# Kernel optimization log

Measured on AMD Instinct MI355X. Metric: run time of the kernel, lower is better.

Reference implementation:

```python
import jax, jax.numpy as jnp
import numpy as np

B, C, H, W = 16, 1536, 32, 32
K = 64      # num_clusters
D = 128     # cluster_dim
T = 256     # token_dim
E = 2       # num_experts
SINK_ITERS = 3


def _l2n(x, axis):
    return x / jnp.maximum(jnp.linalg.norm(x, axis=axis, keepdims=True), 1e-12)


def setup_inputs() -> dict:
    key = jax.random.key(0)
    ks = jax.random.split(key, 16)
    w = lambda k, sh: (jax.random.normal(k, sh, jnp.float32) * 0.02)
    inp = {
        "x_feat": jax.random.normal(ks[0], (B, C, H, W), jnp.float32),
        "token": jax.random.normal(ks[1], (B, C), jnp.float32),
        # cluster_features: Conv1x1 C->512, ReLU, Conv1x1 512->D
        "cf_w1": w(ks[2], (512, C)), "cf_b1": jnp.zeros((512,), jnp.float32),
        "cf_w2": w(ks[3], (D, 512)), "cf_b2": jnp.zeros((D,), jnp.float32),
        # token_features: Linear C->512, ReLU, Linear 512->T
        "tf_w1": w(ks[4], (512, C)), "tf_b1": jnp.zeros((512,), jnp.float32),
        "tf_w2": w(ks[5], (T, 512)), "tf_b2": jnp.zeros((T,), jnp.float32),
        # MoE experts (stacked): Conv1x1 C->512, ReLU, Conv1x1 512->K
        "ex_w1": w(ks[6], (E, 512, C)), "ex_b1": jnp.zeros((E, 512), jnp.float32),
        "ex_w2": w(ks[7], (E, K, 512)), "ex_b2": jnp.zeros((E, K), jnp.float32),
        # gate: Linear C->128, ReLU, Linear 128->E
        "g_w1": w(ks[8], (128, C)), "g_b1": jnp.zeros((128,), jnp.float32),
        "g_w2": w(ks[9], (E, 128)), "g_b2": jnp.zeros((E,), jnp.float32),
        "dust_bin": jnp.array(1.0, jnp.float32),
    }
    return inp


def _log_optimal_transport(scores, alpha, iters):
    b, m, n = scores.shape
    ms, ns = jnp.float32(m), jnp.float32(n)
    bins = jnp.broadcast_to(alpha, (b, 1, n))
    Z = jnp.concatenate([scores, bins], axis=1)          # [b, m+1, n]
    norm = -jnp.log(ms + ns)
    log_mu = jnp.concatenate([jnp.full((m,), norm), (jnp.log(ns) + norm)[None]])
    log_nu = jnp.full((n,), norm)
    u = jnp.zeros((b, m + 1), Z.dtype)
    v = jnp.zeros((b, n), Z.dtype)
    for _ in range(iters):
        u = log_mu[None] - jax.nn.logsumexp(Z + v[:, None, :], axis=2)
        v = log_nu[None] - jax.nn.logsumexp(Z + u[:, :, None], axis=1)
    return Z + u[:, :, None] + v[:, None, :] - norm


def reference(x_feat, token, cf_w1, cf_b1, cf_w2, cf_b2, tf_w1, tf_b1, tf_w2,
              tf_b2, ex_w1, ex_b1, ex_w2, ex_b2, g_w1, g_b1, g_w2, g_b2,
              dust_bin):
    # dropout layers act as identity at inference
    xf = x_feat.reshape(B, C, H * W)                     # [B,C,N]
    # cluster features f: [B, D, N]
    h = jax.nn.relu(jnp.einsum('bcn,oc->bon', xf, cf_w1) + cf_b1[None, :, None])
    f = jnp.einsum('bon,do->bdn', h, cf_w2) + cf_b2[None, :, None]
    # MoE score p: [B, K, N]
    eh = jax.nn.relu(jnp.einsum('bcn,eoc->ebon', xf, ex_w1) + ex_b1[:, None, :, None])
    eo = jnp.einsum('ebon,eko->ebkn', eh, ex_w2) + ex_b2[:, None, :, None]
    g = jax.nn.relu(token @ g_w1.T + g_b1) @ g_w2.T + g_b2   # [B,E]
    gw = jax.nn.softmax(g, axis=1)
    p = jnp.einsum('be,ebkn->bkn', gw, eo)
    # token features t: [B, T]
    t = jax.nn.relu(token @ tf_w1.T + tf_b1) @ tf_w2.T + tf_b2
    # optimal transport + aggregation
    Z = _log_optimal_transport(p, dust_bin, SINK_ITERS)
    P = jnp.exp(Z)[:, :-1, :]                            # [B,K,N]
    agg = jnp.einsum('bdn,bkn->bdk', f, P)               # == (f*p).sum(-1)
    local = _l2n(agg, axis=1).reshape(B, D * K)
    out = jnp.concatenate([_l2n(t, axis=-1), local], axis=-1)
    return _l2n(out, axis=-1)
```

## Files before the change

### kernel.cpp

```cpp
#include <hip/hip_runtime.h>
#include <hip/hip_bf16.h>
#include <math.h>

#define B_  16
#define C_  1536
#define N_  1024
#define K_  64
#define D_  128
#define T_  256
#define OUTW (T_ + D_*K_)

typedef __attribute__((ext_vector_type(8))) short short8_t;
typedef __attribute__((ext_vector_type(4))) float f32x4;

__device__ __forceinline__ ushort f2bf(float f){
  union { float f; uint u; } x; x.f = f;
  return (ushort)((x.u + 0x7fffu + ((x.u >> 16) & 1u)) >> 16);
}

__device__ __forceinline__ void gload16(const ushort* g, ushort* l){
  __builtin_amdgcn_global_load_lds((const __attribute__((address_space(1))) void*)g,
                                   (__attribute__((address_space(3))) void*)l, 16, 0, 0);
}

__global__ __launch_bounds__(256) void k_prep_w(
    const float* __restrict__ cf_w1, const float* __restrict__ ex_w1,
    ushort* __restrict__ Wbf)
{
  size_t i = ((size_t)blockIdx.x*256 + threadIdx.x) * 8;
  const float* src = (i < (size_t)512*C_) ? (cf_w1 + i) : (ex_w1 + (i - (size_t)512*C_));
  float4 a = *(const float4*)(src);
  float4 b = *(const float4*)(src + 4);
  uint4 ov;
  ov.x = (uint)f2bf(a.x) | ((uint)f2bf(a.y) << 16);
  ov.y = (uint)f2bf(a.z) | ((uint)f2bf(a.w) << 16);
  ov.z = (uint)f2bf(b.x) | ((uint)f2bf(b.y) << 16);
  ov.w = (uint)f2bf(b.z) | ((uint)f2bf(b.w) << 16);
  *(uint4*)(Wbf + i) = ov;
}

__global__ __launch_bounds__(256) void k_prep_w2(
    const float* __restrict__ cf_w2, const float* __restrict__ ex_w2,
    ushort* __restrict__ W2bf)
{
  size_t i = ((size_t)blockIdx.x*256 + threadIdx.x) * 8;
  const float* src = (i < (size_t)65536) ? (cf_w2 + i) : (ex_w2 + (i - 65536));
  float4 a = *(const float4*)(src);
  float4 b = *(const float4*)(src + 4);
  uint4 ov;
  ov.x = (uint)f2bf(a.x) | ((uint)f2bf(a.y) << 16);
  ov.y = (uint)f2bf(a.z) | ((uint)f2bf(a.w) << 16);
  ov.z = (uint)f2bf(b.x) | ((uint)f2bf(b.y) << 16);
  ov.w = (uint)f2bf(b.z) | ((uint)f2bf(b.w) << 16);
  *(uint4*)(W2bf + i) = ov;
}

__global__ __launch_bounds__(256) void k_prep_x(
    const float* __restrict__ x, ushort* __restrict__ xT, int b0)
{
  const int bx = blockIdx.x;
  const int by = blockIdx.y;
  const int bz = blockIdx.z;
  const int t  = threadIdx.x;
  __shared__ float Ls[64][65];
  const float* xb = x + (size_t)(bz + b0)*C_*N_ + (size_t)by*64*N_ + bx*64;
  const int r  = t >> 4;
  const int cq = (t & 15) * 4;
  #pragma unroll
  for (int p = 0; p < 4; p++) {
    float4 v = *(const float4*)(xb + (size_t)(r + p*16)*N_ + cq);
    Ls[r + p*16][cq+0] = v.x; Ls[r + p*16][cq+1] = v.y;
    Ls[r + p*16][cq+2] = v.z; Ls[r + p*16][cq+3] = v.w;
  }
  __syncthreads();
  ushort* xTb = xT + ((size_t)bz*N_ + (size_t)bx*64)*C_ + by*64;
  const int rn = t >> 3;
  const int cc = (t & 7) * 8;
  #pragma unroll
  for (int p = 0; p < 2; p++) {
    int n = rn + p*32;
    uint4 ov;
    ov.x = (uint)f2bf(Ls[cc+0][n]) | ((uint)f2bf(Ls[cc+1][n]) << 16);
    ov.y = (uint)f2bf(Ls[cc+2][n]) | ((uint)f2bf(Ls[cc+3][n]) << 16);
    ov.z = (uint)f2bf(Ls[cc+4][n]) | ((uint)f2bf(Ls[cc+5][n]) << 16);
    ov.w = (uint)f2bf(Ls[cc+6][n]) | ((uint)f2bf(Ls[cc+7][n]) << 16);
    *(uint4*)(xTb + (size_t)n*C_ + cc) = ov;
  }
}

__global__ __launch_bounds__(256) void k_token_a(
    const float* __restrict__ token,
    const float* __restrict__ tf_w1, const float* __restrict__ tf_b1,
    const float* __restrict__ g_w1, const float* __restrict__ g_b1,
    float* __restrict__ th1, float* __restrict__ gh)
{
  const int b = blockIdx.y;
  const int o = blockIdx.x*4 + (threadIdx.x >> 6);
  const int lane = threadIdx.x & 63;
  const float* w; float bias; float* dst;
  if (o < 512) { w = tf_w1 + (size_t)o*C_; bias = tf_b1[o]; dst = th1 + b*512 + o; }
  else { int oo = o - 512; w = g_w1 + (size_t)oo*C_; bias = g_b1[oo]; dst = gh + b*128 + oo; }
  const float* tok = token + (size_t)b*C_;
  float s = 0.f;
  for (int c = lane; c < C_; c += 64) s = fmaf(tok[c], w[c], s);
  for (int off = 32; off; off >>= 1) s += __shfl_down(s, off);
  if (lane == 0) *dst = fmaxf(s + bias, 0.f);
}

__global__ __launch_bounds__(256) void k_token_b(
    const float* __restrict__ th1, const float* __restrict__ gh,
    const float* __restrict__ tf_w2, const float* __restrict__ tf_b2,
    const float* __restrict__ g_w2, const float* __restrict__ g_b2,
    float* __restrict__ tt, float* __restrict__ gw)
{
  const int b = blockIdx.y;
  const int wid = threadIdx.x >> 6, lane = threadIdx.x & 63;
  if (blockIdx.x < 64) {
    const int o = blockIdx.x*4 + wid;
    const float* w = tf_w2 + (size_t)o*512;
    const float* h = th1 + b*512;
    float s = 0.f;
    for (int c = lane; c < 512; c += 64) s = fmaf(h[c], w[c], s);
    for (int off = 32; off; off >>= 1) s += __shfl_down(s, off);
    if (lane == 0) tt[b*T_ + o] = s + tf_b2[o];
  } else {
    __shared__ float gl[2];
    if (wid < 2) {
      const float* w = g_w2 + wid*128;
      const float* h = gh + b*128;
      float s = 0.f;
      for (int c = lane; c < 128; c += 64) s = fmaf(h[c], w[c], s);
      for (int off = 32; off; off >>= 1) s += __shfl_down(s, off);
      if (lane == 0) gl[wid] = s + g_b2[wid];
    }
    __syncthreads();
    if (threadIdx.x == 0) {
      float m = fmaxf(gl[0], gl[1]);
      float e0 = __expf(gl[0]-m), e1 = __expf(gl[1]-m);
      float inv = 1.f / (e0 + e1);
      gw[b*2+0] = e0*inv; gw[b*2+1] = e1*inv;
    }
  }
}

__global__ __launch_bounds__(256) void k_gemm1(
    const ushort* __restrict__ Wbf, const ushort* __restrict__ xT,
    const float* __restrict__ cf_b1, const float* __restrict__ ex_b1,
    ushort* __restrict__ hT, int b0)
{
  const int bx = blockIdx.x;
  const int by = blockIdx.y;
  const int bz = blockIdx.z;
  const int t = threadIdx.x;
  const int wid = t >> 6, lane = t & 63;
  const int wr = wid >> 1, wc = wid & 1;
  __shared__ ushort Abuf[128*64];
  __shared__ ushort Bbuf[128*64];
  f32x4 acc[4][4];
  const f32x4 z4 = {0.f, 0.f, 0.f, 0.f};
  #pragma unroll
  for (int i = 0; i < 4; i++)
    #pragma unroll
    for (int j = 0; j < 4; j++) acc[i][j] = z4;

  const ushort* gA[4]; const ushort* gB[4];
  ushort* lA[4]; ushort* lB[4];
  #pragma unroll
  for (int j = 0; j < 4; j++) {
    int idx = j*256 + t;
    int row = idx >> 3, ps = idx & 7;
    int s = ps ^ (row & 7);
    gA[j] = Wbf + (size_t)(by*128 + row)*C_ + s*8;
    gB[j] = xT + ((size_t)bz*N_ + bx*128 + row)*C_ + s*8;
    lA[j] = &Abuf[(j*4 + wid)*512];
    lB[j] = &Bbuf[(j*4 + wid)*512];
  }

  for (int k0 = 0; k0 < C_; k0 += 64) {
    #pragma unroll
    for (int j = 0; j < 4; j++) {
      gload16(gA[j] + k0, lA[j]);
      gload16(gB[j] + k0, lB[j]);
    }
    __syncthreads();
    #pragma unroll
    for (int ks = 0; ks < 2; ks++) {
      short8_t a[4], bb[4];
      const int l15 = lane & 15, lg = lane >> 4;
      #pragma unroll
      for (int i = 0; i < 4; i++) {
        int row = wr*64 + i*16 + l15;
        int slot = ks*4 + lg;
        a[i] = *(const short8_t*)&Abuf[row*64 + ((slot ^ (row & 7)) * 8)];
      }
      #pragma unroll
      for (int j = 0; j < 4; j++) {
        int row = wc*64 + j*16 + l15;
        int slot = ks*4 + lg;
        bb[j] = *(const short8_t*)&Bbuf[row*64 + ((slot ^ (row & 7)) * 8)];
      }
      #pragma unroll
      for (int i = 0; i < 4; i++)
        #pragma unroll
        for (int j = 0; j < 4; j++)
          acc[i][j] = __builtin_amdgcn_mfma_f32_16x16x32_bf16(a[i], bb[j], acc[i][j], 0, 0, 0);
    }
    __syncthreads();
  }
  const int lr = lane >> 4, lc = lane & 15;
  #pragma unroll
  for (int i = 0; i < 4; i++) {
    int o4 = by*128 + wr*64 + i*16 + lr*4;
    float4 bi = (o4 < 512) ? *(const float4*)(cf_b1 + o4)
                           : *(const float4*)(ex_b1 + o4 - 512);
    #pragma unroll
    for (int j = 0; j < 4; j++) {
      int n = bx*128 + wc*64 + j*16 + lc;
      f32x4 v = acc[i][j];
      ushort4 pk;
      pk.x = f2bf(fmaxf(v[0] + bi.x, 0.f));
      pk.y = f2bf(fmaxf(v[1] + bi.y, 0.f));
      pk.z = f2bf(fmaxf(v[2] + bi.z, 0.f));
      pk.w = f2bf(fmaxf(v[3] + bi.w, 0.f));
      *(ushort4*)(hT + ((size_t)(b0 + bz)*N_ + n)*1536 + o4) = pk;
    }
  }
}

__global__ __launch_bounds__(256) void k_gemm2f(
    const ushort* __restrict__ W2bf, const ushort* __restrict__ hT,
    const float* __restrict__ cf_b2, float* __restrict__ f)
{
  const int bx = blockIdx.x;
  const int b  = blockIdx.y;
  const int t = threadIdx.x;
  const int wid = t >> 6, lane = t & 63;
  const int wr = wid >> 1, wc = wid & 1;
  __shared__ ushort Abuf[128*64];
  __shared__ ushort Bbuf[128*64];
  f32x4 acc[4][4];
  const f32x4 z4 = {0.f, 0.f, 0.f, 0.f};
  #pragma unroll
  for (int i = 0; i < 4; i++)
    #pragma unroll
    for (int j = 0; j < 4; j++) acc[i][j] = z4;

  const ushort* gA[4]; const ushort* gB[4];
  ushort* lA[4]; ushort* lB[4];
  #pragma unroll
  for (int j = 0; j < 4; j++) {
    int idx = j*256 + t;
    int row = idx >> 3, ps = idx & 7;
    int s = ps ^ (row & 7);
    gA[j] = W2bf + (size_t)row*512 + s*8;
    gB[j] = hT + ((size_t)b*N_ + bx*128 + row)*1536 + s*8;
    lA[j] = &Abuf[(j*4 + wid)*512];
    lB[j] = &Bbuf[(j*4 + wid)*512];
  }

  for (int k0 = 0; k0 < 512; k0 += 64) {
    #pragma unroll
    for (int j = 0; j < 4; j++) {
      gload16(gA[j] + k0, lA[j]);
      gload16(gB[j] + k0, lB[j]);
    }
    __syncthreads();
    #pragma unroll
    for (int ks = 0; ks < 2; ks++) {
      short8_t a[4], bb[4];
      const int l15 = lane & 15, lg = lane >> 4;
      #pragma unroll
      for (int i = 0; i < 4; i++) {
        int row = wr*64 + i*16 + l15;
        int slot = ks*4 + lg;
        a[i] = *(const short8_t*)&Abuf[row*64 + ((slot ^ (row & 7)) * 8)];
      }
      #pragma unroll
      for (int j = 0; j < 4; j++) {
        int row = wc*64 + j*16 + l15;
        int slot = ks*4 + lg;
        bb[j] = *(const short8_t*)&Bbuf[row*64 + ((slot ^ (row & 7)) * 8)];
      }
      #pragma unroll
      for (int i = 0; i < 4; i++)
        #pragma unroll
        for (int j = 0; j < 4; j++)
          acc[i][j] = __builtin_amdgcn_mfma_f32_16x16x32_bf16(a[i], bb[j], acc[i][j], 0, 0, 0);
    }
    __syncthreads();
  }
  const int lr = lane >> 4, lc = lane & 15;
  #pragma unroll
  for (int i = 0; i < 4; i++) {
    int d0 = wr*64 + i*16 + lr*4;
    float4 bi = *(const float4*)(cf_b2 + d0);
    float bia[4] = {bi.x, bi.y, bi.z, bi.w};
    #pragma unroll
    for (int j = 0; j < 4; j++) {
      int n = bx*128 + wc*64 + j*16 + lc;
      f32x4 v = acc[i][j];
      #pragma unroll
      for (int r = 0; r < 4; r++)
        f[((size_t)b*D_ + d0 + r)*N_ + n] = v[r] + bia[r];
    }
  }
}

__global__ __launch_bounds__(256) void k_gemm2p(
    const ushort* __restrict__ W2bf, const ushort* __restrict__ hT,
    const float* __restrict__ ex_b2, const float* __restrict__ gw,
    float* __restrict__ p)
{
  const int bx = blockIdx.x;
  const int b  = blockIdx.y;
  const int t = threadIdx.x;
  const int wid = t >> 6, lane = t & 63;
  const int wr = wid >> 1, wc = wid & 1;
  __shared__ ushort A0[64*64], A1[64*64];
  __shared__ ushort B0[128*64], B1[128*64];
  f32x4 acc0[2][4], acc1[2][4];
  const f32x4 z4 = {0.f, 0.f, 0.f, 0.f};
  #pragma unroll
  for (int i = 0; i < 2; i++)
    #pragma unroll
    for (int j = 0; j < 4; j++) { acc0[i][j] = z4; acc1[i][j] = z4; }

  const ushort* W2p = W2bf + 65536;
  const ushort* gA0[2]; const ushort* gA1[2];
  const ushort* gB0[4]; const ushort* gB1[4];
  ushort *lA0[2], *lA1[2], *lB0[4], *lB1[4];
  #pragma unroll
  for (int j = 0; j < 2; j++) {
    int idx = j*256 + t;
    int row = idx >> 3, ps = idx & 7;
    int s = ps ^ (row & 7);
    gA0[j] = W2p + (size_t)row*512 + s*8;
    gA1[j] = W2p + (size_t)(64 + row)*512 + s*8;
    lA0[j] = &A0[(j*4 + wid)*512];
    lA1[j] = &A1[(j*4 + wid)*512];
  }
  #pragma unroll
  for (int j = 0; j < 4; j++) {
    int idx = j*256 + t;
    int row = idx >> 3, ps = idx & 7;
    int s = ps ^ (row & 7);
    gB0[j] = hT + ((size_t)b*N_ + bx*128 + row)*1536 + 512 + s*8;
    gB1[j] = hT + ((size_t)b*N_ + bx*128 + row)*1536 + 1024 + s*8;
    lB0[j] = &B0[(j*4 + wid)*512];
    lB1[j] = &B1[(j*4 + wid)*512];
  }

  for (int k0 = 0; k0 < 512; k0 += 64) {
    #pragma unroll
    for (int j = 0; j < 2; j++) {
      gload16(gA0[j] + k0, lA0[j]);
      gload16(gA1[j] + k0, lA1[j]);
    }
    #pragma unroll
    for (int j = 0; j < 4; j++) {
      gload16(gB0[j] + k0, lB0[j]);
      gload16(gB1[j] + k0, lB1[j]);
    }
    __syncthreads();
    #pragma unroll
    for (int ks = 0; ks < 2; ks++) {
      short8_t a0[2], a1[2], b0[4], b1[4];
      const int l15 = lane & 15, lg = lane >> 4;
      #pragma unroll
      for (int i = 0; i < 2; i++) {
        int row = wr*32 + i*16 + l15;
        int slot = ks*4 + lg;
        a0[i] = *(const short8_t*)&A0[row*64 + ((slot ^ (row & 7)) * 8)];
        a1[i] = *(const short8_t*)&A1[row*64 + ((slot ^ (row & 7)) * 8)];
      }
      #pragma unroll
      for (int j = 0; j < 4; j++) {
        int row = wc*64 + j*16 + l15;
        int slot = ks*4 + lg;
        b0[j] = *(const short8_t*)&B0[row*64 + ((slot ^ (row & 7)) * 8)];
        b1[j] = *(const short8_t*)&B1[row*64 + ((slot ^ (row & 7)) * 8)];
      }
      #pragma unroll
      for (int i = 0; i < 2; i++)
        #pragma unroll
        for (int j = 0; j < 4; j++) {
          acc0[i][j] = __builtin_amdgcn_mfma_f32_16x16x32_bf16(a0[i], b0[j], acc0[i][j], 0, 0, 0);
          acc1[i][j] = __builtin_amdgcn_mfma_f32_16x16x32_bf16(a1[i], b1[j], acc1[i][j], 0, 0, 0);
        }
    }
    __syncthreads();
  }
  const float gw0 = gw[b*2 + 0], gw1 = gw[b*2 + 1];
  const int lr = lane >> 4, lc = lane & 15;
  #pragma unroll
  for (int i = 0; i < 2; i++) {
    int kr0 = wr*32 + i*16 + lr*4;
    #pragma unroll
    for (int j = 0; j < 4; j++) {
      int n = bx*128 + wc*64 + j*16 + lc;
      f32x4 v0 = acc0[i][j], v1 = acc1[i][j];
      #pragma unroll
      for (int r = 0; r < 4; r++) {
        int kk = kr0 + r;
        float val = gw0*v0[r] + gw1*v1[r] + gw0*ex_b2[kk] + gw1*ex_b2[64 + kk];
        p[((size_t)b*K_ + kk)*N_ + n] = val;
      }
    }
  }
}

__global__ __launch_bounds__(1024) void k_sinkhorn(
    float* __restrict__ p, const float* __restrict__ dust)
{
  const int b = blockIdx.x;
  const int t = threadIdx.x;
  const int wid = t >> 6, lane = t & 63;
  __shared__ float u[65];
  __shared__ float v[N_];
  const float alpha = dust[0];
  const float NORM  = -logf((float)(K_ + N_));
  const float LOGNS = logf((float)N_);
  float* pb = p + (size_t)b*K_*N_;
  v[t] = 0.f;
  __syncthreads();
  for (int it = 0; it < 3; it++) {
    for (int k = wid; k < 65; k += 16) {
      const bool bin = (k == 64);
      float ml = -1e30f, sl = 0.f;
      for (int n = lane; n < N_; n += 64) {
        float z = (bin ? alpha : pb[(size_t)k*N_ + n]) + v[n];
        if (z > ml) { sl = sl * __expf(ml - z) + 1.f; ml = z; }
        else sl += __expf(z - ml);
      }
      for (int off = 32; off; off >>= 1) {
        float mo = __shfl_xor(ml, off);
        float so = __shfl_xor(sl, off);
        float mn = fmaxf(ml, mo);
        sl = sl * __expf(ml - mn) + so * __expf(mo - mn);
        ml = mn;
      }
      if (lane == 0) u[k] = (bin ? (LOGNS + NORM) : NORM) - (ml + __logf(sl));
    }
    __syncthreads();
    {
      float ml = -1e30f, sl = 0.f;
      for (int k = 0; k < 65; k++) {
        float z = ((k < 64) ? pb[(size_t)k*N_ + t] : alpha) + u[k];
        if (z > ml) { sl = sl * __expf(ml - z) + 1.f; ml = z; }
        else sl += __expf(z - ml);
      }
      v[t] = NORM - (ml + __logf(sl));
    }
    __syncthreads();
  }
  for (int k = 0; k < 64; k++) {
    float z = pb[(size_t)k*N_ + t];
    pb[(size_t)k*N_ + t] = __expf(z + u[k] + v[t] - NORM);
  }
}

__global__ __launch_bounds__(256) void k_aggmm(
    const float* __restrict__ f, const float* __restrict__ P,
    float* __restrict__ pagg)
{
  const int nc = blockIdx.x;
  const int b  = blockIdx.y;
  const int t  = threadIdx.x;
  __shared__ float fs[128][129];
  __shared__ float Ps[64][129];
  const float* fb = f + (size_t)b*D_*N_ + nc*128;
  const float* Pb = P + (size_t)b*K_*N_ + nc*128;
  #pragma unroll
  for (int pp = 0; pp < 16; pp++) {
    int flat = pp*256 + t;
    int row = flat >> 5, c4 = (flat & 31)*4;
    float4 v = *(const float4*)(fb + (size_t)row*N_ + c4);
    fs[row][c4+0] = v.x; fs[row][c4+1] = v.y; fs[row][c4+2] = v.z; fs[row][c4+3] = v.w;
  }
  #pragma unroll
  for (int pp = 0; pp < 8; pp++) {
    int flat = pp*256 + t;
    int row = flat >> 5, c4 = (flat & 31)*4;
    float4 v = *(const float4*)(Pb + (size_t)row*N_ + c4);
    Ps[row][c4+0] = v.x; Ps[row][c4+1] = v.y; Ps[row][c4+2] = v.z; Ps[row][c4+3] = v.w;
  }
  __syncthreads();
  const int td = t >> 3;
  const int tk = t & 7;
  float acc[4][8] = {};
  #pragma unroll 4
  for (int nn = 0; nn < 128; nn++) {
    float fv[4], pv[8];
    #pragma unroll
    for (int i = 0; i < 4; i++) fv[i] = fs[td*4 + i][nn];
    #pragma unroll
    for (int j = 0; j < 8; j++) pv[j] = Ps[tk*8 + j][nn];
    #pragma unroll
    for (int i = 0; i < 4; i++)
      #pragma unroll
      for (int j = 0; j < 8; j++)
        acc[i][j] = fmaf(fv[i], pv[j], acc[i][j]);
  }
  float* ob = pagg + (((size_t)b*8 + nc)*128)*64;
  #pragma unroll
  for (int i = 0; i < 4; i++) {
    #pragma unroll
    for (int j = 0; j < 8; j += 4) {
      float4 v = {acc[i][j], acc[i][j+1], acc[i][j+2], acc[i][j+3]};
      *(float4*)(ob + (size_t)(td*4 + i)*64 + tk*8 + j) = v;
    }
  }
}

__global__ __launch_bounds__(1024) void k_finish(
    const float* __restrict__ pagg, const float* __restrict__ tt_g,
    float* __restrict__ out)
{
  const int b = blockIdx.x;
  const int t = threadIdx.x;
  const int wid = t >> 6, lane = t & 63;
  __shared__ float fs[128][65];
  __shared__ float Ps[64][65];
  __shared__ float invk[64];
  __shared__ float redw[16];
  __shared__ float redw2[16];
  __shared__ float tts[256];
  __shared__ float scal[2];
  if (t < 256) tts[t] = tt_g[b*T_ + t];
  {
    const int d = t >> 3, k0 = (t & 7)*8;
    float4 s0 = {0,0,0,0}, s1 = {0,0,0,0};
    #pragma unroll
    for (int c = 0; c < 8; c++) {
      const float* src = pagg + (((size_t)b*8 + c)*128 + d)*64 + k0;
      float4 a = *(const float4*)(src);
      float4 bq = *(const float4*)(src + 4);
      s0.x += a.x; s0.y += a.y; s0.z += a.z; s0.w += a.w;
      s1.x += bq.x; s1.y += bq.y; s1.z += bq.z; s1.w += bq.w;
    }
    fs[d][k0+0] = s0.x; fs[d][k0+1] = s0.y; fs[d][k0+2] = s0.z; fs[d][k0+3] = s0.w;
    fs[d][k0+4] = s1.x; fs[d][k0+5] = s1.y; fs[d][k0+6] = s1.z; fs[d][k0+7] = s1.w;
  }
  __syncthreads();
  { int k = t & 63, dc = t >> 6;
    float s = 0.f;
    for (int d = dc*8; d < dc*8 + 8; d++) { float w = fs[d][k]; s = fmaf(w, w, s); }
    Ps[k][dc] = s; }
  __syncthreads();
  if (t < 64) {
    float s = 0.f;
    for (int dc = 0; dc < 16; dc++) s += Ps[t][dc];
    float inv = 1.f / fmaxf(sqrtf(s), 1e-12f);
    invk[t] = inv;
    Ps[t][16] = s * inv * inv;
  }
  __syncthreads();
  float p1 = 0.f, p2 = 0.f;
  if (t < 64)  p2 = Ps[t][16];
  if (t < T_)  { float w = tts[t]; p1 = w*w; }
  for (int off = 32; off; off >>= 1) { p1 += __shfl_down(p1, off); p2 += __shfl_down(p2, off); }
  if (lane == 0) { redw[wid] = p1; redw2[wid] = p2; }
  __syncthreads();
  if (t == 0) {
    float s1 = 0.f, s2 = 0.f;
    for (int w = 0; w < 16; w++) { s1 += redw[w]; s2 += redw2[w]; }
    float invT = 1.f / fmaxf(sqrtf(s1), 1e-12f);
    float tot  = s1*invT*invT + s2;
    float invG = 1.f / fmaxf(sqrtf(tot), 1e-12f);
    scal[0] = invG;
    scal[1] = invT * invG;
  }
  __syncthreads();
  const float invG = scal[0], invTG = scal[1];
  for (int idx = t; idx < OUTW; idx += 1024) {
    float vv;
    if (idx < T_) vv = tts[idx] * invTG;
    else { int r = idx - T_; int d = r >> 6, k = r & 63; vv = fs[d][k] * invk[k] * invG; }
    out[(size_t)b*OUTW + idx] = vv;
  }
}

extern "C" void kernel_launch(void* const* d_in, const int* in_sizes, int n_in,
                              void* d_out, int out_size, void* d_ws, size_t ws_size,
                              hipStream_t stream)
{
  const float* x_feat = (const float*)d_in[0];
  const float* token  = (const float*)d_in[1];
  const float* cf_w1  = (const float*)d_in[2];
  const float* cf_b1  = (const float*)d_in[3];
  const float* cf_w2  = (const float*)d_in[4];
  const float* cf_b2  = (const float*)d_in[5];
  const float* tf_w1  = (const float*)d_in[6];
  const float* tf_b1  = (const float*)d_in[7];
  const float* tf_w2  = (const float*)d_in[8];
  const float* tf_b2  = (const float*)d_in[9];
  const float* ex_w1  = (const float*)d_in[10];
  const float* ex_b1  = (const float*)d_in[11];
  const float* ex_w2  = (const float*)d_in[12];
  const float* ex_b2  = (const float*)d_in[13];
  const float* g_w1   = (const float*)d_in[14];
  const float* g_b1   = (const float*)d_in[15];
  const float* g_w2   = (const float*)d_in[16];
  const float* g_b2   = (const float*)d_in[17];
  const float* dust   = (const float*)d_in[18];
  float* out = (float*)d_out;

  char* ws = (char*)d_ws;
  float*  tt   = (float*)(ws + 0);
  float*  gw   = (float*)(ws + 65536);
  float*  th1  = (float*)(ws + 131072);
  float*  gh   = (float*)(ws + 262144);
  ushort* Wbf  = (ushort*)(ws + 524288);
  ushort* W2bf = (ushort*)(ws + 5242880);
  ushort* xT   = (ushort*)(ws + 8388608);
  ushort* hT   = (ushort*)(ws + 33554432);
  float*  f    = (float*)(ws + 8388608);
  float*  p    = (float*)(ws + 16777216);
  float*  pagg = (float*)(ws + 25165824);

  k_prep_w<<<dim3(1152), dim3(256), 0, stream>>>(cf_w1, ex_w1, Wbf);
  k_prep_w2<<<dim3(64), dim3(256), 0, stream>>>(cf_w2, ex_w2, W2bf);
  k_token_a<<<dim3(160, 16), dim3(256), 0, stream>>>(token, tf_w1, tf_b1, g_w1, g_b1, th1, gh);
  k_token_b<<<dim3(65, 16), dim3(256), 0, stream>>>(th1, gh, tf_w2, tf_b2, g_w2, g_b2, tt, gw);
  for (int ph = 0; ph < 2; ph++) {
    k_prep_x<<<dim3(16, 24, 8), dim3(256), 0, stream>>>(x_feat, xT, ph*8);
    k_gemm1<<<dim3(8, 12, 8), dim3(256), 0, stream>>>(Wbf, xT, cf_b1, ex_b1, hT, ph*8);
  }
  k_gemm2f<<<dim3(8, 16), dim3(256), 0, stream>>>(W2bf, hT, cf_b2, f);
  k_gemm2p<<<dim3(8, 16), dim3(256), 0, stream>>>(W2bf, hT, ex_b2, gw, p);
  k_sinkhorn<<<dim3(16), dim3(1024), 0, stream>>>(p, dust);
  k_aggmm<<<dim3(8, 16), dim3(256), 0, stream>>>(f, p, pagg);
  k_finish<<<dim3(16), dim3(1024), 0, stream>>>(pagg, tt, out);
}
```

Before: 475.7 us.

## Keep Sinkhorn column scores in registers and use shuffle-reduced plain exp sums

```diff
diff --git a/kernel.cpp b/kernel.cpp
--- a/kernel.cpp
+++ b/kernel.cpp
@@ -416,47 +416,45 @@
   const int t = threadIdx.x;
   const int wid = t >> 6, lane = t & 63;
   __shared__ float u[65];
-  __shared__ float v[N_];
+  __shared__ float part[65][17];
   const float alpha = dust[0];
   const float NORM  = -logf((float)(K_ + N_));
   const float LOGNS = logf((float)N_);
   float* pb = p + (size_t)b*K_*N_;
-  v[t] = 0.f;
-  __syncthreads();
+  float z[64];
+  #pragma unroll
+  for (int k = 0; k < 64; k++) z[k] = pb[(size_t)k*N_ + t];
+  float v = 0.f;
   for (int it = 0; it < 3; it++) {
-    for (int k = wid; k < 65; k += 16) {
-      const bool bin = (k == 64);
-      float ml = -1e30f, sl = 0.f;
-      for (int n = lane; n < N_; n += 64) {
-        float z = (bin ? alpha : pb[(size_t)k*N_ + n]) + v[n];
-        if (z > ml) { sl = sl * __expf(ml - z) + 1.f; ml = z; }
-        else sl += __expf(z - ml);
-      }
-      for (int off = 32; off; off >>= 1) {
-        float mo = __shfl_xor(ml, off);
-        float so = __shfl_xor(sl, off);
-        float mn = fmaxf(ml, mo);
-        sl = sl * __expf(ml - mn) + so * __expf(mo - mn);
-        ml = mn;
-      }
-      if (lane == 0) u[k] = (bin ? (LOGNS + NORM) : NORM) - (ml + __logf(sl));
-    }
-    __syncthreads();
+    #pragma unroll
+    for (int k = 0; k < 64; k++) {
+      float e = __expf(z[k] + v);
+      #pragma unroll
+      for (int off = 32; off; off >>= 1) e += __shfl_xor(e, off);
+      if (lane == 0) part[k][wid] = e;
+    }
     {
-      float ml = -1e30f, sl = 0.f;
-      for (int k = 0; k < 65; k++) {
-        float z = ((k < 64) ? pb[(size_t)k*N_ + t] : alpha) + u[k];
-        if (z > ml) { sl = sl * __expf(ml - z) + 1.f; ml = z; }
-        else sl += __expf(z - ml);
-      }
-      v[t] = NORM - (ml + __logf(sl));
-    }
-    __syncthreads();
-  }
-  for (int k = 0; k < 64; k++) {
-    float z = pb[(size_t)k*N_ + t];
-    pb[(size_t)k*N_ + t] = __expf(z + u[k] + v[t] - NORM);
-  }
+      float e = __expf(alpha + v);
+      #pragma unroll
+      for (int off = 32; off; off >>= 1) e += __shfl_xor(e, off);
+      if (lane == 0) part[64][wid] = e;
+    }
+    __syncthreads();
+    if (t < 65) {
+      float s = 0.f;
+      #pragma unroll
+      for (int w = 0; w < 16; w++) s += part[t][w];
+      u[t] = ((t == 64) ? (LOGNS + NORM) : NORM) - __logf(s);
+    }
+    __syncthreads();
+    float s = __expf(alpha + u[64]);
+    #pragma unroll
+    for (int k = 0; k < 64; k++) s += __expf(z[k] + u[k]);
+    v = NORM - __logf(s);
+  }
+  #pragma unroll
+  for (int k = 0; k < 64; k++)
+    pb[(size_t)k*N_ + t] = __expf(z[k] + u[k] + v - NORM);
 }
 
 __global__ __launch_bounds__(256) void k_aggmm(
```

Measured after the change: 477.4 us. Within noise of the previous version (+0.4%).
